# Optimization experiments

Hardware: AMD Instinct MI355X
Metric: run time of the kernel (lower is better)

## Reference

```python
import jax, jax.numpy as jnp
import numpy as np

VR = 8          # voxel_resolution
CLASSES = 40
LO, HI = -2.0, 2.0


def setup_inputs() -> dict:
    key = jax.random.key(0)
    kx, kw, kb = jax.random.split(key, 3)
    B, N = 1024, 8192
    in_dim = VR ** 3
    x = jax.random.normal(kx, (B, N, 3), dtype=jnp.float32)
    W = jax.random.normal(kw, (CLASSES, in_dim), dtype=jnp.float32) / np.sqrt(in_dim)
    b = jax.random.normal(kb, (CLASSES,), dtype=jnp.float32) * 0.01
    return {"x": x, "W": W, "b": b}


def _voxel_counts(x):
    """Fused equivalent of the per-sample torch.histogramdd loop.

    x: (B, N, 3) in [-2, 2]; uniform bins -> direct index arithmetic +
    one segment_sum over all B*N points. Matches torch.histogramdd
    semantics: points outside [LO, HI] are dropped; x == HI falls in the
    last bin. Returns normalized counts (B, VR**3).
    """
    B, N, _ = x.shape
    width = (HI - LO) / VR
    idx = jnp.floor((x - LO) / width).astype(jnp.int32)      # (B, N, 3)
    idx = jnp.minimum(idx, VR - 1)                            # x == HI -> last bin
    valid = jnp.all((x >= LO) & (x <= HI), axis=-1)           # (B, N)
    lin = (idx[..., 0] * VR + idx[..., 1]) * VR + idx[..., 2]  # (B, N)
    seg = jnp.arange(B, dtype=jnp.int32)[:, None] * (VR ** 3) + lin
    # out-of-range points -> segment id beyond num_segments (dropped)
    seg = jnp.where(valid, seg, B * VR ** 3)
    ones = jnp.ones((B, N), dtype=x.dtype)
    counts = jax.ops.segment_sum(ones.reshape(-1), seg.reshape(-1),
                                 num_segments=B * VR ** 3)
    return counts.reshape(B, VR ** 3) / N


def reference(x, W, b):
    counts = _voxel_counts(x)                 # (B, VR**3)
    # mode == "count": use normalized counts as-is
    return counts @ W.T + b                   # (B, classes)
```

## Files before the change

kernel.cpp:

```cpp
#include <hip/hip_runtime.h>


#define VR      8
#define BINS    512
#define CLASSES 40
#define NPTS    8192
#define THREADS 512
#define NGROUPS 4

__global__ __launch_bounds__(THREADS, 8) void voxel_cls_kernel(
    const float* __restrict__ x,
    const float* __restrict__ W,
    const float* __restrict__ bias,
    float* __restrict__ out)
{
    __shared__ unsigned int hist[BINS];
    const int t = threadIdx.x;
    const int b = blockIdx.x;

    hist[t] = 0u;
    __syncthreads();

    const float4* px = (const float4*)(x + (size_t)b * NPTS * 3);
    #pragma unroll 2
    for (int g = 0; g < NGROUPS; ++g) {
        const int base = (g * THREADS + t) * 3;
        const float4 A = px[base + 0];
        const float4 B = px[base + 1];
        const float4 C = px[base + 2];

        const float qx[4] = {A.x, A.w, B.z, C.y};
        const float qy[4] = {A.y, B.x, B.w, C.z};
        const float qz[4] = {A.z, B.y, C.x, C.w};

        #pragma unroll
        for (int p = 0; p < 4; ++p) {
            const float vx = qx[p], vy = qy[p], vz = qz[p];
            const bool ok = (__builtin_fabsf(vx) <= 2.f) &&
                            (__builtin_fabsf(vy) <= 2.f) &&
                            (__builtin_fabsf(vz) <= 2.f);
            const int ix = min((int)((vx + 2.f) * 2.f), VR - 1);
            const int iy = min((int)((vy + 2.f) * 2.f), VR - 1);
            const int iz = min((int)((vz + 2.f) * 2.f), VR - 1);
            if (ok) {
                const int lin = (ix * VR + iy) * VR + iz;
                atomicAdd(&hist[lin], 1u);
            }
        }
    }
    __syncthreads();

    if (t < CLASSES * 4) {
        const int c = t >> 2;
        const int s = t & 3;
        const float* Wc = W + c * BINS;
        float acc = 0.f;
        #pragma unroll 8
        for (int i = 0; i < BINS / 4; ++i) {
            const int v = i * 4 + s;
            acc += (float)hist[v] * Wc[v];
        }
        acc += __shfl_xor(acc, 1);
        acc += __shfl_xor(acc, 2);
        if (s == 0)
            out[b * CLASSES + c] = acc * (1.0f / NPTS) + bias[c];
    }
}

extern "C" void kernel_launch(void* const* d_in, const int* in_sizes, int n_in,
                              void* d_out, int out_size, void* d_ws, size_t ws_size,
                              hipStream_t stream) {
    const float* x    = (const float*)d_in[0];
    const float* W    = (const float*)d_in[1];
    const float* bias = (const float*)d_in[2];
    float* out        = (float*)d_out;

    const int nbatch = in_sizes[0] / (NPTS * 3);
    voxel_cls_kernel<<<nbatch, THREADS, 0, stream>>>(x, W, bias, out);
}
```

Measured before the change: 154.9 us.

## Stage point chunks through shared memory with register prefetch for coalesced loads

Each block now loads its points in chunks of 2048 using fully coalesced float4 reads into registers, stores them to a shared-memory staging buffer, and prefetches the next chunk while the current one is binned. Each thread reads its points as strided scalar loads from LDS. Before, each thread read three consecutive float4s at a stride of 48 bytes between threads. The change is meant to improve global load coalescing and to overlap the next chunk's load with the atomic histogram work. In exchange it adds 24KB of LDS per block, which may reduce occupancy, plus extra barriers per chunk and LDS traffic.

```diff
diff --git a/kernel.cpp b/kernel.cpp
--- a/kernel.cpp
+++ b/kernel.cpp
@@ -1,12 +1,14 @@
 #include <hip/hip_runtime.h>
 
 
-#define VR      8
-#define BINS    512
-#define CLASSES 40
-#define NPTS    8192
-#define THREADS 512
-#define NGROUPS 4
+#define VR        8
+#define BINS      512
+#define CLASSES   40
+#define NPTS      8192
+#define THREADS   512
+#define CHUNK_PTS 2048
+#define CHUNK_F4  1536
+#define NCHUNK    4
 
 __global__ __launch_bounds__(THREADS, 8) void voxel_cls_kernel(
     const float* __restrict__ x,
@@ -14,38 +16,44 @@
     const float* __restrict__ bias,
     float* __restrict__ out)
 {
+    __shared__ float xs[CHUNK_PTS * 3];
     __shared__ unsigned int hist[BINS];
     const int t = threadIdx.x;
     const int b = blockIdx.x;
 
     hist[t] = 0u;
-    __syncthreads();
 
     const float4* px = (const float4*)(x + (size_t)b * NPTS * 3);
-    #pragma unroll 2
-    for (int g = 0; g < NGROUPS; ++g) {
-        const int base = (g * THREADS + t) * 3;
-        const float4 A = px[base + 0];
-        const float4 B = px[base + 1];
-        const float4 C = px[base + 2];
+    float4* xsv = (float4*)xs;
 
-        const float qx[4] = {A.x, A.w, B.z, C.y};
-        const float qy[4] = {A.y, B.x, B.w, C.z};
-        const float qz[4] = {A.z, B.y, C.x, C.w};
+    float4 r0 = px[t];
+    float4 r1 = px[t + 512];
+    float4 r2 = px[t + 1024];
+
+    for (int c = 0; c < NCHUNK; ++c) {
+        __syncthreads();
+        xsv[t]        = r0;
+        xsv[t + 512]  = r1;
+        xsv[t + 1024] = r2;
+        if (c + 1 < NCHUNK) {
+            const float4* ns = px + (c + 1) * CHUNK_F4;
+            r0 = ns[t]; r1 = ns[t + 512]; r2 = ns[t + 1024];
+        }
+        __syncthreads();
 
         #pragma unroll
-        for (int p = 0; p < 4; ++p) {
-            const float vx = qx[p], vy = qy[p], vz = qz[p];
+        for (int k = 0; k < 4; ++k) {
+            const int p = k * THREADS + t;
+            const float vx = xs[p * 3 + 0];
+            const float vy = xs[p * 3 + 1];
+            const float vz = xs[p * 3 + 2];
             const bool ok = (__builtin_fabsf(vx) <= 2.f) &&
                             (__builtin_fabsf(vy) <= 2.f) &&
                             (__builtin_fabsf(vz) <= 2.f);
             const int ix = min((int)((vx + 2.f) * 2.f), VR - 1);
             const int iy = min((int)((vy + 2.f) * 2.f), VR - 1);
             const int iz = min((int)((vz + 2.f) * 2.f), VR - 1);
-            if (ok) {
-                const int lin = (ix * VR + iy) * VR + iz;
-                atomicAdd(&hist[lin], 1u);
-            }
+            if (ok) atomicAdd(&hist[(ix * VR + iy) * VR + iz], 1u);
         }
     }
     __syncthreads();
```

Result: no change. 153.7 us (-0.8%).
